# Performance work log

Measured on AMD Instinct MI355X. Metric: run time of the kernel, lower is better.

## Reference

```python
import jax, jax.numpy as jnp
import numpy as np

N = 2048      # nodes per graph
Q = 9         # output_dim (emotion nodes)
D = 256       # input_dim == hidden_dim
L = 4         # num_layers - 1 GIN layers
B = 32        # batch
E = 32768     # edges per graph
EPS = 1e-5    # BatchNorm eps


def _bn(x, g, b, m, v):
    # eval-mode BatchNorm1d over last (channel) dim
    return (x - m) * (g * jax.lax.rsqrt(v + EPS)) + b


def setup_inputs() -> dict:
    key = jax.random.key(0)
    ks = jax.random.split(key, 18)
    s = 1.0 / np.sqrt(D)
    return {
        "batch_feature": jax.random.normal(ks[0], (B, N, D), jnp.float32),
        "edge_mat": jax.random.randint(ks[1], (2, E), 0, N, dtype=jnp.int32),
        "emotion_emb": jax.random.normal(ks[2], (1, Q, D), jnp.float32) * 0.05,
        "mlp_w1": jax.random.normal(ks[3], (L, D, D), jnp.float32) * s,
        "mlp_b1": jnp.zeros((L, D), jnp.float32),
        "mlp_bn_g": jnp.ones((L, D), jnp.float32),
        "mlp_bn_b": jnp.zeros((L, D), jnp.float32),
        "mlp_bn_m": jax.random.normal(ks[4], (L, D), jnp.float32) * 0.1,
        "mlp_bn_v": jax.random.uniform(ks[5], (L, D), jnp.float32, 0.5, 1.5),
        "mlp_w2": jax.random.normal(ks[6], (L, D, D), jnp.float32) * s,
        "mlp_b2": jnp.zeros((L, D), jnp.float32),
        "bn_g": jnp.ones((L, D), jnp.float32),
        "bn_b": jnp.zeros((L, D), jnp.float32),
        "bn_m": jax.random.normal(ks[7], (L, D), jnp.float32) * 0.1,
        "bn_v": jax.random.uniform(ks[8], (L, D), jnp.float32, 0.5, 1.5),
        "pred_w": jax.random.normal(ks[9], (L + 1, D), jnp.float32) * s,
        "pred_b": jnp.zeros((L + 1,), jnp.float32),
    }


def reference(batch_feature, edge_mat, emotion_emb, mlp_w1, mlp_b1,
              mlp_bn_g, mlp_bn_b, mlp_bn_m, mlp_bn_v, mlp_w2, mlp_b2,
              bn_g, bn_b, bn_m, bn_v, pred_w, pred_b):
    # overwrite first Q node rows with shared emotion embeddings
    h = batch_feature.at[:, :Q, :].set(emotion_emb)          # [B, N, D]
    src, dst = edge_mat[0], edge_mat[1]

    def spmm(x):
        # Adj @ x with self-loops; graph topology shared across batch.
        gathered = x[:, dst, :]                              # [B, E, D]
        agg = jax.vmap(
            lambda g: jax.ops.segment_sum(g, src, num_segments=N)
        )(gathered)                                          # [B, N, D]
        return agg + x  # self-loop (identity added to adjacency)

    hidden = [h]
    for l in range(L):
        pooled = spmm(h)
        # 2-layer GIN MLP: Linear -> BN -> ReLU -> Linear
        t = jnp.einsum('bnd,de->bne', pooled, mlp_w1[l]) + mlp_b1[l]
        t = jax.nn.relu(_bn(t, mlp_bn_g[l], mlp_bn_b[l], mlp_bn_m[l], mlp_bn_v[l]))
        t = jnp.einsum('bnd,de->bne', t, mlp_w2[l]) + mlp_b2[l]
        # outer BatchNorm + ReLU
        h = jax.nn.relu(_bn(t, bn_g[l], bn_b[l], bn_m[l], bn_v[l]))
        hidden.append(h)

    score = jnp.zeros((B, Q), jnp.float32)
    for l, hl in enumerate(hidden):
        h_emotion = hl[:, :Q, :]                             # [B, Q, D]
        score = score + jnp.einsum('bqd,d->bq', h_emotion, pred_w[l]) + pred_b[l]
    return jax.nn.sigmoid(score)                             # [B, Q]
```

## Files before the change

kernel.cpp:

```cpp
#include <hip/hip_runtime.h>
#include <hip/hip_bf16.h>

#define NN 2048
#define QQ 9
#define DD 256
#define LL 4
#define BB 32
#define EE 32768
#define EPSV 1e-5f

typedef __attribute__((ext_vector_type(8))) short bf16x8;
typedef __attribute__((ext_vector_type(8))) ushort u16x8;
typedef __attribute__((ext_vector_type(4))) float f32x4;
typedef __attribute__((ext_vector_type(2))) float f32x2;
typedef __attribute__((ext_vector_type(4))) int i32x4;

__device__ __forceinline__ ushort f2bf(float x)
{
    uint u = __float_as_uint(x);
    u += 0x7FFFu + ((u >> 16) & 1u);
    return (ushort)(u >> 16);
}
__device__ __forceinline__ float bf2f(ushort h)
{
    return __uint_as_float(((uint)h) << 16);
}

__device__ __forceinline__ void addw(uint wd, f32x2& a)
{
    f32x2 v;
    v.x = __uint_as_float(wd << 16);
    v.y = __uint_as_float(wd & 0xffff0000u);
    a += v;
}

__device__ __forceinline__ void gload16(const ushort* g, ushort* l)
{
    __builtin_amdgcn_global_load_lds(
        (const __attribute__((address_space(1))) void*)g,
        (__attribute__((address_space(3))) void*)l, 16, 0, 0);
}

__global__ void k_count(const int* __restrict__ src, int* __restrict__ cnt)
{
    int e = blockIdx.x * blockDim.x + threadIdx.x;
    if (e < EE) atomicAdd(&cnt[src[e]], 1);
}

__global__ __launch_bounds__(256) void k_scan(const int* __restrict__ cnt,
                                              int* __restrict__ row_ptr,
                                              int* __restrict__ cursor)
{
    __shared__ int part[256];
    int t = threadIdx.x;
    int local[8];
    int s = 0;
    #pragma unroll
    for (int i = 0; i < 8; ++i) { local[i] = cnt[t * 8 + i]; s += local[i]; }
    part[t] = s;
    __syncthreads();
    for (int off = 1; off < 256; off <<= 1) {
        int v = (t >= off) ? part[t - off] : 0;
        __syncthreads();
        part[t] += v;
        __syncthreads();
    }
    int run = part[t] - s;
    #pragma unroll
    for (int i = 0; i < 8; ++i) {
        int idx = t * 8 + i;
        row_ptr[idx] = run;
        cursor[idx]  = run;
        run += local[i];
    }
    if (t == 255) row_ptr[NN] = run;
}

__global__ void k_fill(const int* __restrict__ src, const int* __restrict__ dst,
                       int* __restrict__ cursor, int* __restrict__ col)
{
    int e = blockIdx.x * blockDim.x + threadIdx.x;
    if (e < EE) {
        int p = atomicAdd(&cursor[src[e]], 1);
        col[p] = dst[e];
    }
}

__global__ void k_prep0(const float4* __restrict__ bf, const float4* __restrict__ emo,
                        ushort4* __restrict__ hhi)
{
    int total = BB * NN * (DD / 4);
    for (int idx = blockIdx.x * blockDim.x + threadIdx.x; idx < total;
         idx += gridDim.x * blockDim.x) {
        int d4 = idx & 63;
        int n  = (idx >> 6) & (NN - 1);
        float4 v = (n < QQ) ? emo[n * 64 + d4] : bf[idx];
        ushort4 h;
        h.x = f2bf(v.x); h.y = f2bf(v.y); h.z = f2bf(v.z); h.w = f2bf(v.w);
        hhi[idx] = h;
    }
}

__global__ __launch_bounds__(256) void k_spmm6(
    const ushort* __restrict__ phi,
    const int* __restrict__ row_ptr, const int* __restrict__ col,
    ushort* __restrict__ ohi)
{
    int x     = blockIdx.x & 7;
    int local = blockIdx.x >> 3;
    int w     = threadIdx.x >> 6;
    int t     = threadIdx.x & 63;
    int inst  = local * 4 + w;
    int pl    = inst >> 11;
    int n     = inst & (NN - 1);
    int b     = x * 4 + pl * 2 + (t >> 5);
    int q     = t & 31;
    const uint* base = (const uint*)(phi + (size_t)b * NN * DD) + q * 4;

    f32x2 a[4];
    {
        uint4 sv = *(const uint4*)(base + (size_t)n * 128);
        a[0] = (f32x2)0.f; a[1] = (f32x2)0.f; a[2] = (f32x2)0.f; a[3] = (f32x2)0.f;
        addw(sv.x, a[0]); addw(sv.y, a[1]); addw(sv.z, a[2]); addw(sv.w, a[3]);
    }

    int beg = row_ptr[n], end = row_ptr[n + 1];
    int j = beg;
    for (; j < end && (j & 3); ++j) {
        uint4 g = *(const uint4*)(base + (size_t)col[j] * 128);
        addw(g.x, a[0]); addw(g.y, a[1]); addw(g.z, a[2]); addw(g.w, a[3]);
    }
    for (; j + 8 <= end; j += 8) {
        i32x4 c0 = *(const i32x4*)(col + j);
        i32x4 c1 = *(const i32x4*)(col + j + 4);
        uint4 g[8];
        g[0] = *(const uint4*)(base + (size_t)c0.x * 128);
        g[1] = *(const uint4*)(base + (size_t)c0.y * 128);
        g[2] = *(const uint4*)(base + (size_t)c0.z * 128);
        g[3] = *(const uint4*)(base + (size_t)c0.w * 128);
        g[4] = *(const uint4*)(base + (size_t)c1.x * 128);
        g[5] = *(const uint4*)(base + (size_t)c1.y * 128);
        g[6] = *(const uint4*)(base + (size_t)c1.z * 128);
        g[7] = *(const uint4*)(base + (size_t)c1.w * 128);
        #pragma unroll
        for (int u = 0; u < 8; ++u) {
            addw(g[u].x, a[0]); addw(g[u].y, a[1]);
            addw(g[u].z, a[2]); addw(g[u].w, a[3]);
        }
    }
    if (j + 4 <= end) {
        i32x4 c = *(const i32x4*)(col + j);
        uint4 g[4];
        g[0] = *(const uint4*)(base + (size_t)c.x * 128);
        g[1] = *(const uint4*)(base + (size_t)c.y * 128);
        g[2] = *(const uint4*)(base + (size_t)c.z * 128);
        g[3] = *(const uint4*)(base + (size_t)c.w * 128);
        #pragma unroll
        for (int u = 0; u < 4; ++u) {
            addw(g[u].x, a[0]); addw(g[u].y, a[1]);
            addw(g[u].z, a[2]); addw(g[u].w, a[3]);
        }
        j += 4;
    }
    for (; j < end; ++j) {
        uint4 g = *(const uint4*)(base + (size_t)col[j] * 128);
        addw(g.x, a[0]); addw(g.y, a[1]); addw(g.z, a[2]); addw(g.w, a[3]);
    }

    u16x8 o;
    #pragma unroll
    for (int k = 0; k < 4; ++k) {
        o[2 * k]     = f2bf(a[k].x);
        o[2 * k + 1] = f2bf(a[k].y);
    }
    *(u16x8*)(ohi + ((size_t)b * NN + n) * DD + q * 8) = o;
}

__global__ __launch_bounds__(256) void k_wprep(const float* __restrict__ w1,
                                               const float* __restrict__ w2,
                                               ushort* __restrict__ wt_hi)
{
    __shared__ float tile[32][36];
    int bx = blockIdx.x;
    int mat = bx >> 6;
    int tt  = bx & 63;
    int tk = (tt >> 3) * 32;
    int tn = (tt & 7) * 32;
    const float* src = (mat < 4) ? (w1 + (size_t)mat * DD * DD)
                                 : (w2 + (size_t)(mat - 4) * DD * DD);
    int t = threadIdx.x;
    int r = t >> 3, c0 = (t & 7) * 4;
    float4 v = *(const float4*)(src + (size_t)(tk + r) * DD + tn + c0);
    tile[r][c0 + 0] = v.x; tile[r][c0 + 1] = v.y;
    tile[r][c0 + 2] = v.z; tile[r][c0 + 3] = v.w;
    __syncthreads();
    int nn = t >> 3, kq = (t & 7) * 4;
    ushort4 hh;
    hh.x = f2bf(tile[kq + 0][nn]); hh.y = f2bf(tile[kq + 1][nn]);
    hh.z = f2bf(tile[kq + 2][nn]); hh.w = f2bf(tile[kq + 3][nn]);
    size_t off = (size_t)mat * DD * DD + (size_t)(tn + nn) * DD + tk + kq;
    *(ushort4*)(wt_hi + off) = hh;
}

__global__ __launch_bounds__(256) void k_gemm_fused(
    const ushort* __restrict__ A, const ushort* __restrict__ W1t,
    const ushort* __restrict__ W2t,
    const float* __restrict__ b1, const float* __restrict__ g1,
    const float* __restrict__ be1, const float* __restrict__ m1,
    const float* __restrict__ v1,
    const float* __restrict__ b2, const float* __restrict__ g2,
    const float* __restrict__ be2, const float* __restrict__ m2,
    const float* __restrict__ v2,
    const float* __restrict__ pw, const float* __restrict__ pb, int l,
    ushort* __restrict__ O, float* __restrict__ out)
{
    __shared__ alignas(16) ushort As[2][64 * 32];
    __shared__ alignas(16) ushort Ws[2][256 * 32];
    __shared__ alignas(16) ushort Ts[64][264];

    int tid = threadIdx.x;
    int x  = blockIdx.x & 7;
    int lm = blockIdx.x >> 3;
    int m0 = x * 8192 + lm * 64;
    int lane = tid & 63;
    int w = tid >> 6;
    int wm = w & 1, wn = w >> 1;
    int lr = lane & 15, kg = lane >> 4;
    int rg = lane >> 4;
    int kgp = kg ^ ((lr >> 1) & 3);

    int sc   = (lane & 3) ^ ((lane >> 3) & 3);
    int srow = lane >> 2;
    const ushort* Aglob = A + (size_t)(m0 + w * 16 + srow) * DD + sc * 8;

    f32x4 acc[2][8];
    #pragma unroll
    for (int m = 0; m < 2; ++m)
        #pragma unroll
        for (int n = 0; n < 8; ++n) acc[m][n] = (f32x4)0.f;

    {
        gload16(Aglob, &As[0][w * 512]);
        #pragma unroll
        for (int i = 0; i < 4; ++i) {
            int seg = i * 4 + w;
            gload16(W1t + (size_t)(seg * 16 + srow) * DD + sc * 8, &Ws[0][seg * 512]);
        }
    }
    int cur = 0;
    for (int kc = 0; kc < 8; ++kc) {
        __syncthreads();
        if (kc < 7) {
            int ko = (kc + 1) * 32;
            gload16(Aglob + ko, &As[cur ^ 1][w * 512]);
            #pragma unroll
            for (int i = 0; i < 4; ++i) {
                int seg = i * 4 + w;
                gload16(W1t + (size_t)(seg * 16 + srow) * DD + ko + sc * 8,
                        &Ws[cur ^ 1][seg * 512]);
            }
        }
        bf16x8 ah[2], bh[8];
        #pragma unroll
        for (int mi = 0; mi < 2; ++mi)
            ah[mi] = *(const bf16x8*)&As[cur][(wm * 32 + mi * 16 + lr) * 32 + kgp * 8];
        #pragma unroll
        for (int n = 0; n < 8; ++n)
            bh[n] = *(const bf16x8*)&Ws[cur][(wn * 128 + n * 16 + lr) * 32 + kgp * 8];
        #pragma unroll
        for (int mi = 0; mi < 2; ++mi)
            #pragma unroll
            for (int n = 0; n < 8; ++n)
                acc[mi][n] = __builtin_amdgcn_mfma_f32_16x16x32_bf16(
                    ah[mi], bh[n], acc[mi][n], 0, 0, 0);
        cur ^= 1;
    }
    {
        float sN[8], svN[8];
        #pragma unroll
        for (int n = 0; n < 8; ++n) {
            int jj = wn * 128 + n * 16 + lr;
            sN[n]  = g1[jj] * rsqrtf(v1[jj] + EPSV);
            svN[n] = (b1[jj] - m1[jj]) * sN[n] + be1[jj];
        }
        #pragma unroll
        for (int m = 0; m < 2; ++m)
            #pragma unroll
            for (int n = 0; n < 8; ++n) {
                int cc = wn * 128 + n * 16 + lr;
                #pragma unroll
                for (int r = 0; r < 4; ++r) {
                    float y = acc[m][n][r] * sN[n] + svN[n];
                    Ts[wm * 32 + m * 16 + rg * 4 + r][cc] = f2bf(y > 0.f ? y : 0.f);
                }
            }
    }
    #pragma unroll
    for (int m = 0; m < 2; ++m)
        #pragma unroll
        for (int n = 0; n < 8; ++n) acc[m][n] = (f32x4)0.f;

    {
        #pragma unroll
        for (int i = 0; i < 4; ++i) {
            int seg = i * 4 + w;
            gload16(W2t + (size_t)(seg * 16 + srow) * DD + sc * 8, &Ws[0][seg * 512]);
        }
    }
    cur = 0;
    for (int kc = 0; kc < 8; ++kc) {
        __syncthreads();
        if (kc < 7) {
            int ko = (kc + 1) * 32;
            #pragma unroll
            for (int i = 0; i < 4; ++i) {
                int seg = i * 4 + w;
                gload16(W2t + (size_t)(seg * 16 + srow) * DD + ko + sc * 8,
                        &Ws[cur ^ 1][seg * 512]);
            }
        }
        bf16x8 a2[2], bh[8];
        #pragma unroll
        for (int mi = 0; mi < 2; ++mi)
            a2[mi] = *(const bf16x8*)&Ts[wm * 32 + mi * 16 + lr][kc * 32 + kg * 8];
        #pragma unroll
        for (int n = 0; n < 8; ++n)
            bh[n] = *(const bf16x8*)&Ws[cur][(wn * 128 + n * 16 + lr) * 32 + kgp * 8];
        #pragma unroll
        for (int mi = 0; mi < 2; ++mi)
            #pragma unroll
            for (int n = 0; n < 8; ++n)
                acc[mi][n] = __builtin_amdgcn_mfma_f32_16x16x32_bf16(
                    a2[mi], bh[n], acc[mi][n], 0, 0, 0);
        cur ^= 1;
    }
    __syncthreads();

    {
        float sN[8], svN[8];
        #pragma unroll
        for (int n = 0; n < 8; ++n) {
            int jj = wn * 128 + n * 16 + lr;
            sN[n]  = g2[jj] * rsqrtf(v2[jj] + EPSV);
            svN[n] = (b2[jj] - m2[jj]) * sN[n] + be2[jj];
        }
        #pragma unroll
        for (int m = 0; m < 2; ++m)
            #pragma unroll
            for (int n = 0; n < 8; ++n) {
                int cc = wn * 128 + n * 16 + lr;
                #pragma unroll
                for (int r = 0; r < 4; ++r) {
                    float y = acc[m][n][r] * sN[n] + svN[n];
                    Ts[wm * 32 + m * 16 + rg * 4 + r][cc] = f2bf(y > 0.f ? y : 0.f);
                }
            }
        #pragma unroll
        for (int i = 0; i < 8; ++i) {
            int cid = lane + i * 64;
            int row = cid >> 4, c8 = cid & 15;
            u16x8 vv = *(const u16x8*)&Ts[wm * 32 + row][wn * 128 + c8 * 8];
            *(u16x8*)(O + (size_t)(m0 + wm * 32 + row) * DD + wn * 128 + c8 * 8) = vv;
        }
    }

    __syncthreads();
    if ((m0 & (NN - 1)) == 0) {
        int b = m0 >> 11;
        for (int q = w; q < QQ; q += 4) {
            ushort4 hv = *(const ushort4*)&Ts[q][lane * 4];
            const float4 wv = *(const float4*)&pw[(l + 1) * DD + lane * 4];
            float s = bf2f(hv.x) * wv.x + bf2f(hv.y) * wv.y +
                      bf2f(hv.z) * wv.z + bf2f(hv.w) * wv.w;
            #pragma unroll
            for (int off = 32; off > 0; off >>= 1) s += __shfl_down(s, off);
            if (lane == 0) {
                float v = out[b * QQ + q] + s + pb[l + 1];
                out[b * QQ + q] = (l == LL - 1) ? 1.f / (1.f + expf(-v)) : v;
            }
        }
    }
}

__global__ __launch_bounds__(64) void k_score0(const float4* __restrict__ emo,
                                               const float4* __restrict__ pw,
                                               const float* __restrict__ pb,
                                               float* __restrict__ out)
{
    int q = blockIdx.x, t = threadIdx.x;
    float4 e = emo[q * 64 + t], wv = pw[t];
    float s = e.x * wv.x + e.y * wv.y + e.z * wv.z + e.w * wv.w;
    #pragma unroll
    for (int off = 32; off > 0; off >>= 1) s += __shfl_down(s, off);
    if (t == 0) {
        s += pb[0];
        for (int b = 0; b < BB; ++b) out[b * QQ + q] = s;
    }
}

extern "C" void kernel_launch(void* const* d_in, const int* in_sizes, int n_in,
                              void* d_out, int out_size, void* d_ws, size_t ws_size,
                              hipStream_t stream)
{
    const float* batch = (const float*)d_in[0];
    const int*   edges = (const int*)d_in[1];
    const float* emo   = (const float*)d_in[2];
    const float* w1    = (const float*)d_in[3];
    const float* b1    = (const float*)d_in[4];
    const float* m_g   = (const float*)d_in[5];
    const float* m_b   = (const float*)d_in[6];
    const float* m_m   = (const float*)d_in[7];
    const float* m_v   = (const float*)d_in[8];
    const float* w2    = (const float*)d_in[9];
    const float* b2    = (const float*)d_in[10];
    const float* g_g   = (const float*)d_in[11];
    const float* g_b   = (const float*)d_in[12];
    const float* g_m   = (const float*)d_in[13];
    const float* g_v   = (const float*)d_in[14];
    const float* pw    = (const float*)d_in[15];
    const float* pb    = (const float*)d_in[16];
    float* out = (float*)d_out;

    const size_t HSZ = (size_t)BB * NN * DD;
    const size_t WT  = (size_t)8 * DD * DD;

    ushort* h_hi = (ushort*)d_ws;
    ushort* P_hi = h_hi + HSZ;
    ushort* wt_hi = P_hi + HSZ;
    int* cnt     = (int*)(wt_hi + WT);
    int* row_ptr = cnt + NN;
    int* cursor  = row_ptr + (NN + 4);
    int* col     = cursor + NN;

    const int* src = edges;
    const int* dst = edges + EE;

    (void)hipMemsetAsync(cnt, 0, NN * sizeof(int), stream);
    k_count<<<EE / 256, 256, 0, stream>>>(src, cnt);
    k_scan<<<1, 256, 0, stream>>>(cnt, row_ptr, cursor);
    k_fill<<<EE / 256, 256, 0, stream>>>(src, dst, cursor, col);
    k_wprep<<<512, 256, 0, stream>>>(w1, w2, wt_hi);
    k_prep0<<<4096, 256, 0, stream>>>((const float4*)batch, (const float4*)emo,
                                      (ushort4*)h_hi);
    k_score0<<<QQ, 64, 0, stream>>>((const float4*)emo, (const float4*)pw, pb, out);

    for (int l = 0; l < LL; ++l) {
        k_spmm6<<<8192, 256, 0, stream>>>(h_hi, row_ptr, col, P_hi);
        k_gemm_fused<<<1024, 256, 0, stream>>>(
            P_hi,
            wt_hi + (size_t)l * DD * DD, wt_hi + (size_t)(4 + l) * DD * DD,
            b1 + l * DD, m_g + l * DD, m_b + l * DD, m_m + l * DD, m_v + l * DD,
            b2 + l * DD, g_g + l * DD, g_b + l * DD, g_m + l * DD, g_v + l * DD,
            pw, pb, l,
            h_hi, out);
    }
}
```

Before: 310.5 us.

## Load full A tile up front and triple-buffer weight chunks in fused GEMM

The fused two-GEMM kernel now loads the whole 64x256 A tile into shared memory at the start, using an XOR swizzle, and reuses that buffer for the intermediate activation tile. Weight K-chunks are triple-buffered with prefetch distance two, synchronised by explicit vmcnt waits and raw s_barrier calls. The aim is to overlap global loads with MFMA work, cut stalls on full __syncthreads, and avoid bank conflicts. Shared memory per block grows to 80 KB, which may reduce occupancy, and the hand-written waitcnt logic adds correctness risk.

```diff
diff --git a/kernel.cpp b/kernel.cpp
--- a/kernel.cpp
+++ b/kernel.cpp
@@ -214,9 +214,8 @@
     const float* __restrict__ pw, const float* __restrict__ pb, int l,
     ushort* __restrict__ O, float* __restrict__ out)
 {
-    __shared__ alignas(16) ushort As[2][64 * 32];
-    __shared__ alignas(16) ushort Ws[2][256 * 32];
-    __shared__ alignas(16) ushort Ts[64][264];
+    __shared__ alignas(16) ushort SM[40960];
+    ushort* AT = SM;
 
     int tid = threadIdx.x;
     int x  = blockIdx.x & 7;
@@ -231,7 +230,26 @@
 
     int sc   = (lane & 3) ^ ((lane >> 3) & 3);
     int srow = lane >> 2;
-    const ushort* Aglob = A + (size_t)(m0 + w * 16 + srow) * DD + sc * 8;
+
+    #pragma unroll
+    for (int i = 0; i < 8; ++i) {
+        int row = (w * 8 + i) * 2 + (lane >> 5);
+        int pc  = lane & 31;
+        int lc  = pc ^ (row & 7);
+        gload16(A + (size_t)(m0 + row) * DD + lc * 8, AT + (w * 8 + i) * 512);
+    }
+    #pragma unroll
+    for (int i = 0; i < 4; ++i) {
+        int seg = i * 4 + w;
+        gload16(W1t + (size_t)(seg * 16 + srow) * DD + sc * 8,
+                SM + 16384 + seg * 512);
+    }
+    #pragma unroll
+    for (int i = 0; i < 4; ++i) {
+        int seg = i * 4 + w;
+        gload16(W1t + (size_t)(seg * 16 + srow) * DD + 32 + sc * 8,
+                SM + 16384 + 8192 + seg * 512);
+    }
 
     f32x4 acc[2][8];
     #pragma unroll
@@ -239,49 +257,129 @@
         #pragma unroll
         for (int n = 0; n < 8; ++n) acc[m][n] = (f32x4)0.f;
 
-    {
-        gload16(Aglob, &As[0][w * 512]);
-        #pragma unroll
-        for (int i = 0; i < 4; ++i) {
-            int seg = i * 4 + w;
-            gload16(W1t + (size_t)(seg * 16 + srow) * DD + sc * 8, &Ws[0][seg * 512]);
-        }
-    }
-    int cur = 0;
+    #pragma unroll
     for (int kc = 0; kc < 8; ++kc) {
-        __syncthreads();
-        if (kc < 7) {
-            int ko = (kc + 1) * 32;
-            gload16(Aglob + ko, &As[cur ^ 1][w * 512]);
+        if (kc < 7) asm volatile("s_waitcnt vmcnt(4)" ::: "memory");
+        else        asm volatile("s_waitcnt vmcnt(0)" ::: "memory");
+        __builtin_amdgcn_sched_barrier(0);
+        __builtin_amdgcn_s_barrier();
+        __builtin_amdgcn_sched_barrier(0);
+        if (kc < 6) {
+            int ko = (kc + 2) * 32;
+            int bi = (kc + 2) % 3;
             #pragma unroll
             for (int i = 0; i < 4; ++i) {
                 int seg = i * 4 + w;
                 gload16(W1t + (size_t)(seg * 16 + srow) * DD + ko + sc * 8,
-                        &Ws[cur ^ 1][seg * 512]);
+                        SM + 16384 + bi * 8192 + seg * 512);
             }
         }
+        const ushort* Wb = SM + 16384 + (kc % 3) * 8192;
         bf16x8 ah[2], bh[8];
         #pragma unroll
-        for (int mi = 0; mi < 2; ++mi)
-            ah[mi] = *(const bf16x8*)&As[cur][(wm * 32 + mi * 16 + lr) * 32 + kgp * 8];
+        for (int mi = 0; mi < 2; ++mi) {
+            int row = wm * 32 + mi * 16 + lr;
+            ah[mi] = *(const bf16x8*)&AT[row * 256 + (((kc * 4 + kg) ^ (row & 7)) * 8)];
+        }
         #pragma unroll
         for (int n = 0; n < 8; ++n)
-            bh[n] = *(const bf16x8*)&Ws[cur][(wn * 128 + n * 16 + lr) * 32 + kgp * 8];
+            bh[n] = *(const bf16x8*)&Wb[(wn * 128 + n * 16 + lr) * 32 + kgp * 8];
         #pragma unroll
         for (int mi = 0; mi < 2; ++mi)
             #pragma unroll
             for (int n = 0; n < 8; ++n)
                 acc[mi][n] = __builtin_amdgcn_mfma_f32_16x16x32_bf16(
                     ah[mi], bh[n], acc[mi][n], 0, 0, 0);
-        cur ^= 1;
-    }
+    }
+    __builtin_amdgcn_s_barrier();
+    __builtin_amdgcn_sched_barrier(0);
+
+    float sN[8], svN[8];
+    #pragma unroll
+    for (int n = 0; n < 8; ++n) {
+        int jj = wn * 128 + n * 16 + lr;
+        sN[n]  = g1[jj] * rsqrtf(v1[jj] + EPSV);
+        svN[n] = (b1[jj] - m1[jj]) * sN[n] + be1[jj];
+    }
+    #pragma unroll
+    for (int i = 0; i < 4; ++i) {
+        int seg = i * 4 + w;
+        gload16(W2t + (size_t)(seg * 16 + srow) * DD + sc * 8,
+                SM + 16384 + seg * 512);
+    }
+    #pragma unroll
+    for (int i = 0; i < 4; ++i) {
+        int seg = i * 4 + w;
+        gload16(W2t + (size_t)(seg * 16 + srow) * DD + 32 + sc * 8,
+                SM + 16384 + 8192 + seg * 512);
+    }
+    #pragma unroll
+    for (int m = 0; m < 2; ++m)
+        #pragma unroll
+        for (int n = 0; n < 8; ++n) {
+            int cc = wn * 128 + n * 16 + lr;
+            #pragma unroll
+            for (int r = 0; r < 4; ++r) {
+                int row = wm * 32 + m * 16 + rg * 4 + r;
+                float y = acc[m][n][r] * sN[n] + svN[n];
+                AT[row * 256 + ((((cc >> 3) ^ (row & 7)) << 3) | (cc & 7))] =
+                    f2bf(y > 0.f ? y : 0.f);
+            }
+        }
+    #pragma unroll
+    for (int m = 0; m < 2; ++m)
+        #pragma unroll
+        for (int n = 0; n < 8; ++n) acc[m][n] = (f32x4)0.f;
+
+    asm volatile("s_waitcnt lgkmcnt(0)" ::: "memory");
+    __builtin_amdgcn_sched_barrier(0);
+    __builtin_amdgcn_s_barrier();
+    __builtin_amdgcn_sched_barrier(0);
+
+    #pragma unroll
+    for (int kc = 0; kc < 8; ++kc) {
+        if (kc < 7) asm volatile("s_waitcnt vmcnt(4)" ::: "memory");
+        else        asm volatile("s_waitcnt vmcnt(0)" ::: "memory");
+        __builtin_amdgcn_sched_barrier(0);
+        __builtin_amdgcn_s_barrier();
+        __builtin_amdgcn_sched_barrier(0);
+        if (kc < 6) {
+            int ko = (kc + 2) * 32;
+            int bi = (kc + 2) % 3;
+            #pragma unroll
+            for (int i = 0; i < 4; ++i) {
+                int seg = i * 4 + w;
+                gload16(W2t + (size_t)(seg * 16 + srow) * DD + ko + sc * 8,
+                        SM + 16384 + bi * 8192 + seg * 512);
+            }
+        }
+        const ushort* Wb = SM + 16384 + (kc % 3) * 8192;
+        bf16x8 ah[2], bh[8];
+        #pragma unroll
+        for (int mi = 0; mi < 2; ++mi) {
+            int row = wm * 32 + mi * 16 + lr;
+            ah[mi] = *(const bf16x8*)&AT[row * 256 + (((kc * 4 + kg) ^ (row & 7)) * 8)];
+        }
+        #pragma unroll
+        for (int n = 0; n < 8; ++n)
+            bh[n] = *(const bf16x8*)&Wb[(wn * 128 + n * 16 + lr) * 32 + kgp * 8];
+        #pragma unroll
+        for (int mi = 0; mi < 2; ++mi)
+            #pragma unroll
+            for (int n = 0; n < 8; ++n)
+                acc[mi][n] = __builtin_amdgcn_mfma_f32_16x16x32_bf16(
+                    ah[mi], bh[n], acc[mi][n], 0, 0, 0);
+    }
+    __builtin_amdgcn_s_barrier();
+    __builtin_amdgcn_sched_barrier(0);
+
     {
-        float sN[8], svN[8];
+        float sN2[8], svN2[8];
         #pragma unroll
         for (int n = 0; n < 8; ++n) {
             int jj = wn * 128 + n * 16 + lr;
-            sN[n]  = g1[jj] * rsqrtf(v1[jj] + EPSV);
-            svN[n] = (b1[jj] - m1[jj]) * sN[n] + be1[jj];
+            sN2[n]  = g2[jj] * rsqrtf(v2[jj] + EPSV);
+            svN2[n] = (b2[jj] - m2[jj]) * sN2[n] + be2[jj];
         }
         #pragma unroll
         for (int m = 0; m < 2; ++m)
@@ -290,85 +388,32 @@
                 int cc = wn * 128 + n * 16 + lr;
                 #pragma unroll
                 for (int r = 0; r < 4; ++r) {
-                    float y = acc[m][n][r] * sN[n] + svN[n];
-                    Ts[wm * 32 + m * 16 + rg * 4 + r][cc] = f2bf(y > 0.f ? y : 0.f);
+                    int row = wm * 32 + m * 16 + rg * 4 + r;
+                    float y = acc[m][n][r] * sN2[n] + svN2[n];
+                    AT[row * 256 + ((((cc >> 3) ^ (row & 7)) << 3) | (cc & 7))] =
+                        f2bf(y > 0.f ? y : 0.f);
                 }
             }
-    }
-    #pragma unroll
-    for (int m = 0; m < 2; ++m)
-        #pragma unroll
-        for (int n = 0; n < 8; ++n) acc[m][n] = (f32x4)0.f;
-
-    {
-        #pragma unroll
-        for (int i = 0; i < 4; ++i) {
-            int seg = i * 4 + w;
-            gload16(W2t + (size_t)(seg * 16 + srow) * DD + sc * 8, &Ws[0][seg * 512]);
-        }
-    }
-    cur = 0;
-    for (int kc = 0; kc < 8; ++kc) {
-        __syncthreads();
-        if (kc < 7) {
-            int ko = (kc + 1) * 32;
-            #pragma unroll
-            for (int i = 0; i < 4; ++i) {
-                int seg = i * 4 + w;
-                gload16(W2t + (size_t)(seg * 16 + srow) * DD + ko + sc * 8,
-                        &Ws[cur ^ 1][seg * 512]);
-            }
-        }
-        bf16x8 a2[2], bh[8];
-        #pragma unroll
-        for (int mi = 0; mi < 2; ++mi)
-            a2[mi] = *(const bf16x8*)&Ts[wm * 32 + mi * 16 + lr][kc * 32 + kg * 8];
-        #pragma unroll
-        for (int n = 0; n < 8; ++n)
-            bh[n] = *(const bf16x8*)&Ws[cur][(wn * 128 + n * 16 + lr) * 32 + kgp * 8];
-        #pragma unroll
-        for (int mi = 0; mi < 2; ++mi)
-            #pragma unroll
-            for (int n = 0; n < 8; ++n)
-                acc[mi][n] = __builtin_amdgcn_mfma_f32_16x16x32_bf16(
-                    a2[mi], bh[n], acc[mi][n], 0, 0, 0);
-        cur ^= 1;
-    }
-    __syncthreads();
-
-    {
-        float sN[8], svN[8];
-        #pragma unroll
-        for (int n = 0; n < 8; ++n) {
-            int jj = wn * 128 + n * 16 + lr;
-            sN[n]  = g2[jj] * rsqrtf(v2[jj] + EPSV);
-            svN[n] = (b2[jj] - m2[jj]) * sN[n] + be2[jj];
-        }
-        #pragma unroll
-        for (int m = 0; m < 2; ++m)
-            #pragma unroll
-            for (int n = 0; n < 8; ++n) {
-                int cc = wn * 128 + n * 16 + lr;
-                #pragma unroll
-                for (int r = 0; r < 4; ++r) {
-                    float y = acc[m][n][r] * sN[n] + svN[n];
-                    Ts[wm * 32 + m * 16 + rg * 4 + r][cc] = f2bf(y > 0.f ? y : 0.f);
-                }
-            }
+        asm volatile("s_waitcnt lgkmcnt(0)" ::: "memory");
+        __builtin_amdgcn_sched_barrier(0);
+        __builtin_amdgcn_s_barrier();
+        __builtin_amdgcn_sched_barrier(0);
         #pragma unroll
         for (int i = 0; i < 8; ++i) {
-            int cid = lane + i * 64;
-            int row = cid >> 4, c8 = cid & 15;
-            u16x8 vv = *(const u16x8*)&Ts[wm * 32 + row][wn * 128 + c8 * 8];
-            *(u16x8*)(O + (size_t)(m0 + wm * 32 + row) * DD + wn * 128 + c8 * 8) = vv;
-        }
-    }
-
-    __syncthreads();
+            int cid = tid + i * 256;
+            int row = cid >> 5;
+            int ci  = cid & 31;
+            u16x8 vv = *(const u16x8*)&AT[row * 256 + ((ci ^ (row & 7)) * 8)];
+            *(u16x8*)(O + (size_t)(m0 + row) * DD + ci * 8) = vv;
+        }
+    }
+
     if ((m0 & (NN - 1)) == 0) {
         int b = m0 >> 11;
         for (int q = w; q < QQ; q += 4) {
-            ushort4 hv = *(const ushort4*)&Ts[q][lane * 4];
+            int chunk = lane >> 1;
+            int phys  = chunk ^ (q & 7);
+            ushort4 hv = *(const ushort4*)&AT[q * 256 + phys * 8 + (lane & 1) * 4];
             const float4 wv = *(const float4*)&pw[(l + 1) * DD + lane * 4];
             float s = bf2f(hv.x) * wv.x + bf2f(hv.y) * wv.y +
                       bf2f(hv.z) * wv.z + bf2f(hv.w) * wv.w;
```

Result: no change. 312.5 us (+0.6%).
